# Optimization experiments

Measured on AMD Instinct MI355X. Metric: run time of the kernel, lower is better.

## Reference

```python
import jax, jax.numpy as jnp
import numpy as np

L = 3          # GRU layers
H = 512        # hidden_dim == latent_dim == atom_vocab_size (required for source to run)
V = 512        # atom_vocab_size
B = 16
S = 96


def setup_inputs() -> dict:
    key = jax.random.key(0)
    ks = jax.random.split(key, 16)
    p = lambda k, shape: jax.random.normal(k, shape, dtype=jnp.float32) * 0.05
    return {
        "z": jax.random.normal(ks[0], (B, H), dtype=jnp.float32),
        "W_l2h": p(ks[1], (H, H)), "b_l2h": p(ks[2], (H,)),
        # GRU weights, torch gate order (r, z, n); stored [in, 3H] so x @ W
        "W_ih": p(ks[3], (L, H, 3 * H)), "W_hh": p(ks[4], (L, H, 3 * H)),
        "b_ih": p(ks[5], (L, 3 * H)), "b_hh": p(ks[6], (L, 3 * H)),
        # atom predictor MLP
        "Wa1": p(ks[7], (H, H)), "ba1": p(ks[8], (H,)),
        "Wa2": p(ks[9], (H, V)), "ba2": p(ks[10], (V,)),
        # bond predictor MLP (in = 2*V = 2*H)
        "Wb1": p(ks[11], (2 * H, H)), "bb1": p(ks[12], (H,)),
        "Wb2": p(ks[13], (H, 4)), "bb2": p(ks[14], (4,)),
        "target_length": S,
    }


def _gru_cell(hl, x, Wih_l, Whh_l, bih_l, bhh_l):
    gi = x @ Wih_l + bih_l          # [B, 3H]
    gh = hl @ Whh_l + bhh_l         # [B, 3H]
    ir, iz, inn = jnp.split(gi, 3, axis=-1)
    hr, hz, hn = jnp.split(gh, 3, axis=-1)
    r = jax.nn.sigmoid(ir + hr)
    zg = jax.nn.sigmoid(iz + hz)
    n = jnp.tanh(inn + r * hn)
    return (1.0 - zg) * n + zg * hl


def reference(z, W_l2h, b_l2h, W_ih, W_hh, b_ih, b_hh,
              Wa1, ba1, Wa2, ba2, Wb1, bb1, Wb2, bb2, target_length):
    batch = z.shape[0]
    seq_len = target_length
    h0 = z @ W_l2h + b_l2h                         # [B, H]
    hidden0 = jnp.broadcast_to(h0[None], (L, batch, H))  # repeat over layers

    x0 = jnp.zeros((batch, H), dtype=z.dtype)      # decoder input is zeros each step

    def step(hs, _):
        x = x0
        new = []
        for l in range(L):
            hl = _gru_cell(hs[l], x, W_ih[l], W_hh[l], b_ih[l], b_hh[l])
            new.append(hl)
            x = hl                                  # no inter-layer dropout (eval)
        logits = jax.nn.relu(x @ Wa1 + ba1) @ Wa2 + ba2   # [B, V]
        return jnp.stack(new), logits

    _, atoms = jax.lax.scan(step, hidden0, None, length=seq_len)  # [S, B, V]
    atoms = atoms.transpose(1, 0, 2)                # [B, S, V]
    atom_indices = jnp.argmax(atoms, axis=-1)       # argmax(softmax) == argmax(logits)

    # all-pairs bond MLP, vectorized: split first linear to avoid [B,S,S,2V] concat
    e_i = atoms @ Wb1[:V]                           # [B, S, H] (contribution of atom i)
    e_j = atoms @ Wb1[V:]                           # [B, S, H] (contribution of atom j)
    hp = jax.nn.relu(e_i[:, :, None, :] + e_j[:, None, :, :] + bb1)  # [B, S, S, H]
    edge = hp @ Wb2 + bb2                           # [B, S, S, 4]
    mask = 1.0 - jnp.eye(seq_len, dtype=edge.dtype)  # i == j entries stay zero
    edge = edge * mask[None, :, :, None]
    return atom_indices, edge
```

## Files before the change

kernel.cpp:

```cpp
#include <hip/hip_runtime.h>
#include <math.h>

#define H    512
#define TH3  1536
#define GRID 224

#define WS_STATE(l,p) ((size_t)((l)*3+(p)) * 8192)
#define WS_A1(p)      ((size_t)73728 + (size_t)(p)*8192)
#define WS_ATOMS      ((size_t)98304)
#define WS_E          ((size_t)884736)

__device__ __forceinline__ float sigm_(float x) { return 1.0f / (1.0f + expf(-x)); }

__device__ __forceinline__ float stampf(float x, unsigned b) {
    return __uint_as_float((__float_as_uint(x) & ~1u) | b);
}
__device__ __forceinline__ int lsb4ok(float4 v, unsigned e) {
    return ((__float_as_uint(v.x) & 1u) == e) & ((__float_as_uint(v.y) & 1u) == e) &
           ((__float_as_uint(v.z) & 1u) == e) & ((__float_as_uint(v.w) & 1u) == e);
}

__device__ __forceinline__ void ld_coh4(const float* p0, const float* p1,
                                        const float* p2, const float* p3,
                                        float4& a, float4& b, float4& c, float4& d)
{
    asm volatile(
        "global_load_dwordx4 %0, %4, off sc0 sc1\n\t"
        "global_load_dwordx4 %1, %5, off sc0 sc1\n\t"
        "global_load_dwordx4 %2, %6, off sc0 sc1\n\t"
        "global_load_dwordx4 %3, %7, off sc0 sc1\n\t"
        "s_waitcnt vmcnt(0)"
        : "=&v"(a), "=&v"(b), "=&v"(c), "=&v"(d)
        : "v"(p0), "v"(p1), "v"(p2), "v"(p3)
        : "memory");
}

__device__ __forceinline__ void ld_coh8(const float* p0, const float* p1,
                                        const float* p2, const float* p3,
                                        const float* p4, const float* p5,
                                        const float* p6, const float* p7,
                                        float4& a, float4& b, float4& c, float4& d,
                                        float4& e, float4& f, float4& g, float4& h)
{
    asm volatile(
        "global_load_dwordx4 %0, %8, off sc0 sc1\n\t"
        "global_load_dwordx4 %1, %9, off sc0 sc1\n\t"
        "global_load_dwordx4 %2, %10, off sc0 sc1\n\t"
        "global_load_dwordx4 %3, %11, off sc0 sc1\n\t"
        "global_load_dwordx4 %4, %12, off sc0 sc1\n\t"
        "global_load_dwordx4 %5, %13, off sc0 sc1\n\t"
        "global_load_dwordx4 %6, %14, off sc0 sc1\n\t"
        "global_load_dwordx4 %7, %15, off sc0 sc1\n\t"
        "s_waitcnt vmcnt(0)"
        : "=&v"(a), "=&v"(b), "=&v"(c), "=&v"(d),
          "=&v"(e), "=&v"(f), "=&v"(g), "=&v"(h)
        : "v"(p0), "v"(p1), "v"(p2), "v"(p3),
          "v"(p4), "v"(p5), "v"(p6), "v"(p7)
        : "memory");
}

__device__ __forceinline__ void st_coh1(float* p, float v) {
    asm volatile("global_store_dword %0, %1, off sc0 sc1" :: "v"(p), "v"(v) : "memory");
}

__device__ __forceinline__ void ld_coh_u32x2(const unsigned* p0, const unsigned* p1,
                                             unsigned& a, unsigned& b)
{
    asm volatile(
        "global_load_dword %0, %2, off sc0 sc1\n\t"
        "global_load_dword %1, %3, off sc0 sc1\n\t"
        "s_waitcnt vmcnt(0)"
        : "=&v"(a), "=&v"(b)
        : "v"(p0), "v"(p1)
        : "memory");
}

__device__ __forceinline__ void st_coh_u32(unsigned* p, unsigned v) {
    asm volatile("global_store_dword %0, %1, off sc0 sc1" :: "v"(p), "v"(v) : "memory");
}

__device__ __forceinline__ void vm_drain() {
    asm volatile("s_waitcnt vmcnt(0)" ::: "memory");
}

template<int CTRL>
__device__ __forceinline__ float dppmov(float v) {
    return __int_as_float(__builtin_amdgcn_update_dpp(
        0, __float_as_int(v), CTRL, 0xF, 0xF, true));
}
#define DPP_XOR1 0xB1
#define DPP_XOR2 0x4E
#define DPP_XOR8 0x128

template<int PAT>
__device__ __forceinline__ float swzf(float v) {
    return __int_as_float(__builtin_amdgcn_ds_swizzle(__float_as_int(v), PAT));
}
#define SWZ_XOR4  0x101F
#define SWZ_XOR16 0x401F

extern "C" __global__ __launch_bounds__(256)
void k_init(const float* __restrict__ z, const float* __restrict__ Wl2h,
            const float* __restrict__ bl2h, float* __restrict__ ws)
{
    if (blockIdx.x == 0)
        ((unsigned*)(ws + WS_E))[threadIdx.x] = 0u;
    const int t  = threadIdx.x;
    const int jl = t & 15, b = t >> 4;
    const int j  = blockIdx.x * 16 + jl;
    float acc = 0.f;
    #pragma unroll 4
    for (int k = 0; k < H; ++k)
        acc += z[b * H + k] * Wl2h[(size_t)k * H + j];
    acc += bl2h[j];

    const unsigned realLsb[3] = { 1u, 0u, 1u };
    const int preh[3][3] = { { 1, 0, -1 },
                             { -1, 0, 1 },
                             { 0, -1, 1 } };
    const unsigned preA1[3] = { 0u, 1u, 0u };
    #pragma unroll
    for (int l = 0; l < 3; ++l)
        #pragma unroll
        for (int p = 0; p < 3; ++p) {
            float v = (preh[l][p] < 0) ? stampf(acc, realLsb[l])
                                       : __uint_as_float((unsigned)preh[l][p]);
            ws[WS_STATE(l, p) + j * 16 + b] = v;
        }
    #pragma unroll
    for (int p = 0; p < 3; ++p)
        ws[WS_A1(p) + j * 16 + b] = __uint_as_float(preA1[p]);
}

__global__ __launch_bounds__(512, 2)
void k_gru(const float* __restrict__ W_ih, const float* __restrict__ W_hh,
           const float* __restrict__ b_ih, const float* __restrict__ b_hh,
           const float* __restrict__ Wa1,  const float* __restrict__ ba1,
           const float* __restrict__ Wa2,  const float* __restrict__ ba2,
           float* __restrict__ ws)
{
    __shared__ float sx[10240];
    __shared__ float sh[10240];
    __shared__ float red[768];
    unsigned* flags = (unsigned*)(ws + WS_E);

    const int bid = blockIdx.x;
    const int tid = threadIdx.x;

    int job, jbase;
    if      (bid < 32)  { job = 0; jbase = bid * 16; }
    else if (bid < 96)  { job = 1; jbase = (bid - 32) * 8; }
    else if (bid < 160) { job = 2; jbase = (bid - 96) * 8; }
    else if (bid < 192) { job = 3; jbase = (bid - 160) * 16; }
    else                { job = 4; jbase = (bid - 192) * 16; }

    const int ks = tid & 31;
    const int qh = (tid >> 5) & 1;
    const int cs = tid >> 6;

    int rs0, rc0;
    if      (job == 0) { rs0 = 0;   rc0 = 96;  }
    else if (job == 1) { rs0 = 32;  rc0 = 128; }
    else if (job == 2) { rs0 = 96;  rc0 = 96;  }
    else if (job == 3) { rs0 = 192; rc0 = 32;  }
    else               { rs0 = 0;   rc0 = 0;   }
    int fidl[2];
    #pragma unroll
    for (int e = 0; e < 2; ++e) {
        int idx = (tid & 63) + e * 64;
        fidl[e] = (idx < rc0) ? rs0 + idx : bid;
    }

    float w[6][16];
    if (job <= 2) {
        const float* Wsrc;
        int colbase;
        if (job == 0) { Wsrc = W_hh; colbase = jbase + cs * 2; }
        else {
            Wsrc = ((cs & 1) ? W_hh : W_ih) + (size_t)job * H * TH3;
            colbase = jbase + (cs >> 1) * 2;
        }
        #pragma unroll
        for (int f = 0; f < 6; ++f) {
            int g = f >> 1, c = f & 1;
            #pragma unroll
            for (int kk = 0; kk < 16; ++kk)
                w[f][kk] = Wsrc[(size_t)(kk * 32 + ks) * TH3 + g * 512 + colbase + c];
        }
    } else {
        const float* base = (job == 3) ? Wa1 : Wa2;
        int colbase = jbase + cs * 2;
        #pragma unroll
        for (int f = 0; f < 2; ++f)
            #pragma unroll
            for (int kk = 0; kk < 16; ++kk)
                w[f][kk] = base[(size_t)(kk * 32 + ks) * H + colbase + f];
    }

    float c_bi0 = 0, c_bi1 = 0, c_bi2 = 0, c_bh0 = 0, c_bh1 = 0, c_bh2 = 0;
    float hp = 0.f, c_ba = 0.f;
    if (job == 0 && tid < 256) {
        int b = tid & 15, j2 = tid >> 4, jc = jbase + j2;
        c_bi0 = b_ih[jc]; c_bi1 = b_ih[512 + jc]; c_bi2 = b_ih[1024 + jc];
        c_bh0 = b_hh[jc]; c_bh1 = b_hh[512 + jc]; c_bh2 = b_hh[1024 + jc];
        hp = ws[WS_STATE(0, 2) + jc * 16 + b];
    } else if ((job == 1 || job == 2) && tid < 128) {
        int b = tid & 15, j2 = tid >> 4, jc = jbase + j2;
        const float* bi  = b_ih + job * TH3;
        const float* bhh = b_hh + job * TH3;
        c_bi0 = bi[jc]; c_bi1 = bi[512 + jc]; c_bi2 = bi[1024 + jc];
        c_bh0 = bhh[jc]; c_bh1 = bhh[512 + jc]; c_bh2 = bhh[1024 + jc];
        hp = ws[WS_STATE(job, (job + 2) % 3) + jc * 16 + b];
    } else if (job == 3 && tid < 256) {
        c_ba = ba1[jbase + (tid >> 4)];
    } else if (job == 4 && tid < 256) {
        c_ba = ba2[jbase + (tid & 15)];
    }

    const int k0 = tid >> 2;
    const int q4 = (tid & 3) * 4;
    const bool b0 = (ks & 1), b1 = (ks & 2), b3 = (ks & 8), b4 = (ks & 16);

    for (int s = 0; s < 100; ++s) {
        const int rp = (s + 2) % 3, wp = s % 3;
        const int act = (s >= job && s <= 95 + job);

        if (act) {
            const unsigned expb = (unsigned)((s + 1) & 1);

            if (tid < 64 && s >= 2) {
                unsigned lim = (unsigned)(s - 1);
                for (;;) {
                    unsigned v0, v1;
                    ld_coh_u32x2(&flags[fidl[0]], &flags[fidl[1]], v0, v1);
                    int ok = (v0 >= lim) && (v1 >= lim);
                    if (__all(ok)) break;
                    __builtin_amdgcn_s_sleep(1);
                }
            }

            if (job == 1 || job == 2) {
                const float* sA = ws + WS_STATE(job - 1, rp);
                const float* sB = ws + WS_STATE(job, rp);
                float4 xa, xb, xc, xd, ha, hb, hc, hd;
                for (;;) {
                    ld_coh8(sA + 4 * tid, sA + 4 * (tid + 512),
                            sA + 4 * (tid + 1024), sA + 4 * (tid + 1536),
                            sB + 4 * tid, sB + 4 * (tid + 512),
                            sB + 4 * (tid + 1024), sB + 4 * (tid + 1536),
                            xa, xb, xc, xd, ha, hb, hc, hd);
                    int ok = lsb4ok(xa, expb) & lsb4ok(xb, expb) &
                             lsb4ok(xc, expb) & lsb4ok(xd, expb) &
                             lsb4ok(ha, expb) & lsb4ok(hb, expb) &
                             lsb4ok(hc, expb) & lsb4ok(hd, expb);
                    if (__all(ok)) break;
                    __builtin_amdgcn_s_sleep(1);
                }
                *(float4*)&sx[(k0      ) * 20 + q4] = xa;
                *(float4*)&sx[(k0 + 128) * 20 + q4] = xb;
                *(float4*)&sx[(k0 + 256) * 20 + q4] = xc;
                *(float4*)&sx[(k0 + 384) * 20 + q4] = xd;
                *(float4*)&sh[(k0      ) * 20 + q4] = ha;
                *(float4*)&sh[(k0 + 128) * 20 + q4] = hb;
                *(float4*)&sh[(k0 + 256) * 20 + q4] = hc;
                *(float4*)&sh[(k0 + 384) * 20 + q4] = hd;
            } else {
                const float* sA = (job == 0) ? (ws + WS_STATE(0, rp))
                                : (job == 3) ? (ws + WS_STATE(2, rp))
                                             : (ws + WS_A1(rp));
                float4 xa, xb, xc, xd;
                for (;;) {
                    ld_coh4(sA + 4 * tid, sA + 4 * (tid + 512),
                            sA + 4 * (tid + 1024), sA + 4 * (tid + 1536),
                            xa, xb, xc, xd);
                    int ok = lsb4ok(xa, expb) & lsb4ok(xb, expb) &
                             lsb4ok(xc, expb) & lsb4ok(xd, expb);
                    if (__all(ok)) break;
                    __builtin_amdgcn_s_sleep(1);
                }
                *(float4*)&sx[(k0      ) * 20 + q4] = xa;
                *(float4*)&sx[(k0 + 128) * 20 + q4] = xb;
                *(float4*)&sx[(k0 + 256) * 20 + q4] = xc;
                *(float4*)&sx[(k0 + 384) * 20 + q4] = xd;
            }
            __syncthreads();

            const int rowoff = 8 * qh;
            if (job <= 2) {
                const float* arr = (job != 0 && (cs & 1)) ? sh : sx;
                float acc[6][8];
                #pragma unroll
                for (int f = 0; f < 6; ++f)
                    #pragma unroll
                    for (int i = 0; i < 8; ++i) acc[f][i] = 0.f;
                #pragma unroll
                for (int kk = 0; kk < 16; ++kk) {
                    const float* p = arr + (kk * 32 + ks) * 20 + rowoff;
                    float4 v0 = *(const float4*)p;
                    float4 v1 = *(const float4*)(p + 4);
                    #pragma unroll
                    for (int f = 0; f < 6; ++f) {
                        float wv = w[f][kk];
                        acc[f][0] += wv * v0.x; acc[f][1] += wv * v0.y;
                        acc[f][2] += wv * v0.z; acc[f][3] += wv * v0.w;
                        acc[f][4] += wv * v1.x; acc[f][5] += wv * v1.y;
                        acc[f][6] += wv * v1.z; acc[f][7] += wv * v1.w;
                    }
                }
                float a[6];
                #pragma unroll
                for (int f = 0; f < 6; ++f) {
                    float t[4];
                    #pragma unroll
                    for (int j = 0; j < 4; ++j) {
                        float give = b0 ? acc[f][j] : acc[f][j + 4];
                        float recv = dppmov<DPP_XOR1>(give);
                        float keep = b0 ? acc[f][j + 4] : acc[f][j];
                        t[j] = keep + recv;
                    }
                    float u[2];
                    #pragma unroll
                    for (int j = 0; j < 2; ++j) {
                        float give = b1 ? t[j] : t[j + 2];
                        float recv = dppmov<DPP_XOR2>(give);
                        float keep = b1 ? t[j + 2] : t[j];
                        u[j] = keep + recv;
                    }
                    {
                        float give = b3 ? u[0] : u[1];
                        float recv = dppmov<DPP_XOR8>(give);
                        float keep = b3 ? u[1] : u[0];
                        a[f] = keep + recv;
                    }
                }
                #pragma unroll
                for (int f = 0; f < 6; ++f) a[f] += swzf<SWZ_XOR4>(a[f]);
                float r[3];
                #pragma unroll
                for (int i = 0; i < 3; ++i) {
                    float give = b4 ? a[i] : a[i + 3];
                    float recv = swzf<SWZ_XOR16>(give);
                    float keep = b4 ? a[i + 3] : a[i];
                    r[i] = keep + recv;
                }
                if (!(ks & 4)) {
                    int bl = ((ks & 1) << 2) | (ks & 2) | ((ks >> 3) & 1);
                    int bb = qh * 8 + bl;
                    int fb3 = ((ks >> 4) & 1) * 3;
                    #pragma unroll
                    for (int i = 0; i < 3; ++i) {
                        int f = fb3 + i, g = f >> 1, c = f & 1;
                        int idx = (job == 0)
                            ? g * 256 + (cs * 2 + c) * 16 + bb
                            : (cs & 1) * 384 + g * 128 + ((cs >> 1) * 2 + c) * 16 + bb;
                        red[idx] = r[i];
                    }
                }
            } else {
                float acc[2][8];
                #pragma unroll
                for (int f = 0; f < 2; ++f)
                    #pragma unroll
                    for (int i = 0; i < 8; ++i) acc[f][i] = 0.f;
                #pragma unroll
                for (int kk = 0; kk < 16; ++kk) {
                    const float* p = sx + (kk * 32 + ks) * 20 + rowoff;
                    float4 v0 = *(const float4*)p;
                    float4 v1 = *(const float4*)(p + 4);
                    #pragma unroll
                    for (int f = 0; f < 2; ++f) {
                        float wv = w[f][kk];
                        acc[f][0] += wv * v0.x; acc[f][1] += wv * v0.y;
                        acc[f][2] += wv * v0.z; acc[f][3] += wv * v0.w;
                        acc[f][4] += wv * v1.x; acc[f][5] += wv * v1.y;
                        acc[f][6] += wv * v1.z; acc[f][7] += wv * v1.w;
                    }
                }
                float a[2];
                #pragma unroll
                for (int f = 0; f < 2; ++f) {
                    float t[4];
                    #pragma unroll
                    for (int j = 0; j < 4; ++j) {
                        float give = b0 ? acc[f][j] : acc[f][j + 4];
                        float recv = dppmov<DPP_XOR1>(give);
                        float keep = b0 ? acc[f][j + 4] : acc[f][j];
                        t[j] = keep + recv;
                    }
                    float u[2];
                    #pragma unroll
                    for (int j = 0; j < 2; ++j) {
                        float give = b1 ? t[j] : t[j + 2];
                        float recv = dppmov<DPP_XOR2>(give);
                        float keep = b1 ? t[j + 2] : t[j];
                        u[j] = keep + recv;
                    }
                    float give = b3 ? u[0] : u[1];
                    float recv = dppmov<DPP_XOR8>(give);
                    float keep = b3 ? u[1] : u[0];
                    a[f] = keep + recv;
                }
                a[0] += swzf<SWZ_XOR4>(a[0]);
                a[1] += swzf<SWZ_XOR4>(a[1]);
                float give = b4 ? a[0] : a[1];
                float recv = swzf<SWZ_XOR16>(give);
                float keep = b4 ? a[1] : a[0];
                float r0 = keep + recv;
                if (!(ks & 4)) {
                    int bl = ((ks & 1) << 2) | (ks & 2) | ((ks >> 3) & 1);
                    int bb = qh * 8 + bl;
                    int fb = (ks >> 4) & 1;
                    red[(cs * 2 + fb) * 16 + bb] = r0;
                }
            }
            __syncthreads();

            const unsigned myb = (unsigned)(s & 1);
            if (job == 0) {
                if (tid < 256) {
                    int b = tid & 15, j2 = tid >> 4, jc = jbase + j2;
                    float g0 = red[       j2 * 16 + b];
                    float g1 = red[256  + j2 * 16 + b];
                    float g2 = red[512  + j2 * 16 + b];
                    float r  = sigm_(c_bi0 + g0 + c_bh0);
                    float zg = sigm_(c_bi1 + g1 + c_bh1);
                    float n  = tanhf(c_bi2 + r * (g2 + c_bh2));
                    float hn = (1.f - zg) * n + zg * hp;
                    hp = hn;
                    st_coh1(&ws[WS_STATE(0, wp) + jc * 16 + b], stampf(hn, myb));
                }
            } else if (job <= 2) {
                if (tid < 128) {
                    int b = tid & 15, j2 = tid >> 4, jc = jbase + j2;
                    float gi0 = red[        j2 * 16 + b], gh0 = red[384 +       j2 * 16 + b];
                    float gi1 = red[128  +  j2 * 16 + b], gh1 = red[384 + 128 + j2 * 16 + b];
                    float gi2 = red[256  +  j2 * 16 + b], gh2 = red[384 + 256 + j2 * 16 + b];
                    float r  = sigm_(gi0 + c_bi0 + gh0 + c_bh0);
                    float zg = sigm_(gi1 + c_bi1 + gh1 + c_bh1);
                    float n  = tanhf(gi2 + c_bi2 + r * (gh2 + c_bh2));
                    float hn = (1.f - zg) * n + zg * hp;
                    hp = hn;
                    st_coh1(&ws[WS_STATE(job, wp) + jc * 16 + b], stampf(hn, myb));
                }
            } else if (job == 3) {
                if (tid < 256) {
                    int b = tid & 15, j2 = tid >> 4, jc = jbase + j2;
                    float v = red[j2 * 16 + b] + c_ba;
                    st_coh1(&ws[WS_A1(wp) + jc * 16 + b], stampf(fmaxf(v, 0.f), myb));
                }
            } else {
                if (tid < 256) {
                    int j2 = tid & 15, b = tid >> 4, jc = jbase + j2;
                    float v = red[j2 * 16 + b] + c_ba;
                    ws[WS_ATOMS + ((size_t)(s - 4) * 16 + b) * H + jc] = v;
                }
            }
        }

        vm_drain();
        __syncthreads();
        if (tid == 0) st_coh_u32(&flags[bid], (unsigned)(s + 1));
    }
}

extern "C" __global__ __launch_bounds__(256)
void k_argmax(const float* __restrict__ ws, float* __restrict__ out)
{
    const int t = blockIdx.x;
    const int wv = threadIdx.x >> 6, lane = threadIdx.x & 63;
    for (int b = wv; b < 16; b += 4) {
        const float* row = ws + WS_ATOMS + ((size_t)t * 16 + b) * H;
        float mx = -3.4028235e38f; int mi = 0;
        #pragma unroll
        for (int c = 0; c < 8; ++c) {
            int idx = lane + c * 64;
            float v = row[idx];
            if (v > mx) { mx = v; mi = idx; }
        }
        #pragma unroll
        for (int off = 32; off >= 1; off >>= 1) {
            float omx = __shfl_down(mx, off);
            int   omi = __shfl_down(mi, off);
            if (omx > mx || (omx == mx && omi < mi)) { mx = omx; mi = omi; }
        }
        if (lane == 0) out[b * 96 + t] = (float)mi;
    }
}

extern "C" __global__ __launch_bounds__(256)
void k_eij(const float* __restrict__ Wb1, const float* __restrict__ bb1,
           float* __restrict__ ws)
{
    __shared__ float aT[8192];
    const int bid = blockIdx.x;
    const int t = bid >> 4, m = (bid >> 3) & 1, ct = bid & 7;
    const int tid = threadIdx.x;
    const float* atoms = ws + WS_ATOMS;
    for (int f = tid; f < 2048; f += 256) {
        int b = f >> 7, kq = f & 127;
        float4 v = ((const float4*)(atoms + ((size_t)(t * 16 + b)) * H))[kq];
        aT[(kq * 4 + 0) * 16 + b] = v.x;
        aT[(kq * 4 + 1) * 16 + b] = v.y;
        aT[(kq * 4 + 2) * 16 + b] = v.z;
        aT[(kq * 4 + 3) * 16 + b] = v.w;
    }
    __syncthreads();
    const int c = tid & 63, rq = tid >> 6;
    const int col = ct * 64 + c;
    const float* Wp = Wb1 + (size_t)m * H * H + col;
    float a0 = 0, a1 = 0, a2 = 0, a3 = 0;
    #pragma unroll 8
    for (int k = 0; k < 512; ++k) {
        float  wv = Wp[(size_t)k * H];
        float4 av = *(const float4*)&aT[k * 16 + rq * 4];
        a0 += av.x * wv; a1 += av.y * wv; a2 += av.z * wv; a3 += av.w * wv;
    }
    float bb = (m == 0) ? bb1[col] : 0.f;
    a0 += bb; a1 += bb; a2 += bb; a3 += bb;
    float* eb = ws + WS_E + (size_t)(m * 16) * 96 * H;
    eb[((size_t)(rq * 4 + 0) * 96 + t) * H + col] = a0;
    eb[((size_t)(rq * 4 + 1) * 96 + t) * H + col] = a1;
    eb[((size_t)(rq * 4 + 2) * 96 + t) * H + col] = a2;
    eb[((size_t)(rq * 4 + 3) * 96 + t) * H + col] = a3;
}

extern "C" __global__ __launch_bounds__(256)
void k_edge(const float* __restrict__ Wb2, const float* __restrict__ bb2,
            const float* __restrict__ ws, float* __restrict__ out)
{
    __shared__ float ls[32][260];
    __shared__ float wsm[2048];
    const int bid = blockIdx.x;
    const int b = bid / 36, r6 = bid % 36, it = r6 / 6, jt = r6 % 6;
    const int tid = threadIdx.x;
    const int ip = tid & 15, jp = tid >> 4;
    float acc0 = 0, acc1 = 0, acc2 = 0, acc3 = 0;

    for (int f = tid; f < 2048; f += 256)
        wsm[f] = Wb2[f];

    for (int ph = 0; ph < 2; ++ph) {
        __syncthreads();
        for (int f = tid; f < 2048; f += 256) {
            int r = f >> 6, c4 = f & 63;
            const float* src = (r < 16)
                ? ws + WS_E + ((size_t)b * 96 + it * 16 + r) * H
                : ws + WS_E + ((size_t)(16 + b) * 96 + jt * 16 + (r - 16)) * H;
            float4 v = *(const float4*)(src + ph * 256 + c4 * 4);
            *(float4*)&ls[r][c4 * 4] = v;
        }
        __syncthreads();
        const float* wb = &wsm[ph * 1024];
        #pragma unroll 2
        for (int hh = 0; hh < 256; hh += 4) {
            float4 ei = *(const float4*)&ls[ip][hh];
            float4 ej = *(const float4*)&ls[16 + jp][hh];
            float4 w0 = *(const float4*)(wb + (size_t)hh * 4);
            float4 w1 = *(const float4*)(wb + (size_t)hh * 4 + 4);
            float4 w2 = *(const float4*)(wb + (size_t)hh * 4 + 8);
            float4 w3 = *(const float4*)(wb + (size_t)hh * 4 + 12);
            float v;
            v = fmaxf(ei.x + ej.x, 0.f); acc0 += v * w0.x; acc1 += v * w0.y; acc2 += v * w0.z; acc3 += v * w0.w;
            v = fmaxf(ei.y + ej.y, 0.f); acc0 += v * w1.x; acc1 += v * w1.y; acc2 += v * w1.z; acc3 += v * w1.w;
            v = fmaxf(ei.z + ej.z, 0.f); acc0 += v * w2.x; acc1 += v * w2.y; acc2 += v * w2.z; acc3 += v * w2.w;
            v = fmaxf(ei.w + ej.w, 0.f); acc0 += v * w3.x; acc1 += v * w3.y; acc2 += v * w3.z; acc3 += v * w3.w;
        }
    }
    const int i = it * 16 + ip, j = jt * 16 + jp;
    float4 o;
    if (i == j) { o.x = 0.f; o.y = 0.f; o.z = 0.f; o.w = 0.f; }
    else { o.x = acc0 + bb2[0]; o.y = acc1 + bb2[1]; o.z = acc2 + bb2[2]; o.w = acc3 + bb2[3]; }
    *(float4*)(out + 1536 + (((size_t)b * 96 + i) * 96 + j) * 4) = o;
}

extern "C" void kernel_launch(void* const* d_in, const int* in_sizes, int n_in,
                              void* d_out, int out_size, void* d_ws, size_t ws_size,
                              hipStream_t stream)
{
    const float* z    = (const float*)d_in[0];
    const float* Wl2h = (const float*)d_in[1];
    const float* bl2h = (const float*)d_in[2];
    const float* W_ih = (const float*)d_in[3];
    const float* W_hh = (const float*)d_in[4];
    const float* b_ih = (const float*)d_in[5];
    const float* b_hh = (const float*)d_in[6];
    const float* Wa1  = (const float*)d_in[7];
    const float* ba1  = (const float*)d_in[8];
    const float* Wa2  = (const float*)d_in[9];
    const float* ba2  = (const float*)d_in[10];
    const float* Wb1  = (const float*)d_in[11];
    const float* bb1  = (const float*)d_in[12];
    const float* Wb2  = (const float*)d_in[13];
    const float* bb2  = (const float*)d_in[14];
    float* out = (float*)d_out;
    float* ws  = (float*)d_ws;

    hipLaunchKernelGGL(k_init, dim3(32), dim3(256), 0, stream, z, Wl2h, bl2h, ws);

    hipLaunchKernelGGL(k_gru, dim3(GRID), dim3(512), 0, stream,
                       W_ih, W_hh, b_ih, b_hh, Wa1, ba1, Wa2, ba2, ws);

    hipLaunchKernelGGL(k_argmax, dim3(96), dim3(256), 0, stream, ws, out);
    hipLaunchKernelGGL(k_eij, dim3(1536), dim3(256), 0, stream, Wb1, bb1, ws);
    hipLaunchKernelGGL(k_edge, dim3(576), dim3(256), 0, stream, Wb2, bb2, ws, out);
}
```

Baseline: 850.1 us.

## Rebalance persistent GRU blocks and prefetch input-layer state one step early

Reassigns the persistent-kernel block roles. Layer 0 now gets 64 blocks of 8 columns, and the atom MLP stages get 16 blocks of 32 columns each. Layers 1 and 2 now stage the previous layer's hidden state into shared memory during the prior iteration, so the input-side matvec can start before the recurrent state arrives. To support this, the per-layer schedule is staggered to 102 steps with new parity stamps and initial buffer patterns, and the reduction buffer is enlarged. The aim is to shorten the critical path of the pipelined recurrence, at the cost of more complex cross-block synchronisation and a longer pipeline fill.

```diff
diff --git a/kernel.cpp b/kernel.cpp
--- a/kernel.cpp
+++ b/kernel.cpp
@@ -35,28 +35,11 @@
         : "memory");
 }
 
-__device__ __forceinline__ void ld_coh8(const float* p0, const float* p1,
-                                        const float* p2, const float* p3,
-                                        const float* p4, const float* p5,
-                                        const float* p6, const float* p7,
-                                        float4& a, float4& b, float4& c, float4& d,
-                                        float4& e, float4& f, float4& g, float4& h)
-{
+__device__ __forceinline__ void ld_coh_u32(const unsigned* p, unsigned& a) {
     asm volatile(
-        "global_load_dwordx4 %0, %8, off sc0 sc1\n\t"
-        "global_load_dwordx4 %1, %9, off sc0 sc1\n\t"
-        "global_load_dwordx4 %2, %10, off sc0 sc1\n\t"
-        "global_load_dwordx4 %3, %11, off sc0 sc1\n\t"
-        "global_load_dwordx4 %4, %12, off sc0 sc1\n\t"
-        "global_load_dwordx4 %5, %13, off sc0 sc1\n\t"
-        "global_load_dwordx4 %6, %14, off sc0 sc1\n\t"
-        "global_load_dwordx4 %7, %15, off sc0 sc1\n\t"
+        "global_load_dword %0, %1, off sc0 sc1\n\t"
         "s_waitcnt vmcnt(0)"
-        : "=&v"(a), "=&v"(b), "=&v"(c), "=&v"(d),
-          "=&v"(e), "=&v"(f), "=&v"(g), "=&v"(h)
-        : "v"(p0), "v"(p1), "v"(p2), "v"(p3),
-          "v"(p4), "v"(p5), "v"(p6), "v"(p7)
-        : "memory");
+        : "=&v"(a) : "v"(p) : "memory");
 }
 
 __device__ __forceinline__ void st_coh1(float* p, float v) {
@@ -114,19 +97,18 @@
         acc += z[b * H + k] * Wl2h[(size_t)k * H + j];
     acc += bl2h[j];
 
-    const unsigned realLsb[3] = { 1u, 0u, 1u };
     const int preh[3][3] = { { 1, 0, -1 },
-                             { -1, 0, 1 },
-                             { 0, -1, 1 } };
-    const unsigned preA1[3] = { 0u, 1u, 0u };
+                             { 0, -1, 1 },
+                             { -1, 1, 0 } };
     #pragma unroll
     for (int l = 0; l < 3; ++l)
         #pragma unroll
         for (int p = 0; p < 3; ++p) {
-            float v = (preh[l][p] < 0) ? stampf(acc, realLsb[l])
+            float v = (preh[l][p] < 0) ? stampf(acc, 1u)
                                        : __uint_as_float((unsigned)preh[l][p]);
             ws[WS_STATE(l, p) + j * 16 + b] = v;
         }
+    const unsigned preA1[3] = { 1u, 0u, 0u };
     #pragma unroll
     for (int p = 0; p < 3; ++p)
         ws[WS_A1(p) + j * 16 + b] = __uint_as_float(preA1[p]);
@@ -141,28 +123,27 @@
 {
     __shared__ float sx[10240];
     __shared__ float sh[10240];
-    __shared__ float red[768];
+    __shared__ float red[1536];
     unsigned* flags = (unsigned*)(ws + WS_E);
 
     const int bid = blockIdx.x;
     const int tid = threadIdx.x;
 
     int job, jbase;
-    if      (bid < 32)  { job = 0; jbase = bid * 16; }
-    else if (bid < 96)  { job = 1; jbase = (bid - 32) * 8; }
-    else if (bid < 160) { job = 2; jbase = (bid - 96) * 8; }
-    else if (bid < 192) { job = 3; jbase = (bid - 160) * 16; }
-    else                { job = 4; jbase = (bid - 192) * 16; }
+    if      (bid < 64)  { job = 0; jbase = bid * 8; }
+    else if (bid < 128) { job = 1; jbase = (bid - 64) * 8; }
+    else if (bid < 192) { job = 2; jbase = (bid - 128) * 8; }
+    else if (bid < 208) { job = 3; jbase = (bid - 192) * 32; }
+    else                { job = 4; jbase = (bid - 208) * 32; }
 
     const int ks = tid & 31;
-    const int qh = (tid >> 5) & 1;
     const int cs = tid >> 6;
 
     int rs0, rc0;
-    if      (job == 0) { rs0 = 0;   rc0 = 96;  }
-    else if (job == 1) { rs0 = 32;  rc0 = 128; }
-    else if (job == 2) { rs0 = 96;  rc0 = 96;  }
-    else if (job == 3) { rs0 = 192; rc0 = 32;  }
+    if      (job == 0) { rs0 = 0;   rc0 = 128; }
+    else if (job == 1) { rs0 = 64;  rc0 = 128; }
+    else if (job == 2) { rs0 = 128; rc0 = 80;  }
+    else if (job == 3) { rs0 = 208; rc0 = 16;  }
     else               { rs0 = 0;   rc0 = 0;   }
     int fidl[2];
     #pragma unroll
@@ -173,25 +154,25 @@
 
     float w[6][16];
     if (job <= 2) {
-        const float* Wsrc;
-        int colbase;
-        if (job == 0) { Wsrc = W_hh; colbase = jbase + cs * 2; }
-        else {
-            Wsrc = ((cs & 1) ? W_hh : W_ih) + (size_t)job * H * TH3;
-            colbase = jbase + (cs >> 1) * 2;
-        }
+        const int khalf = cs & 1, cpair = cs >> 1;
+        const int colbase = jbase + cpair * 2;
+        const float* WB = W_hh + (size_t)job * H * TH3;
+        const float* WA = W_ih + (size_t)job * H * TH3;
         #pragma unroll
         for (int f = 0; f < 6; ++f) {
             int g = f >> 1, c = f & 1;
             #pragma unroll
-            for (int kk = 0; kk < 16; ++kk)
-                w[f][kk] = Wsrc[(size_t)(kk * 32 + ks) * TH3 + g * 512 + colbase + c];
+            for (int kk = 0; kk < 8; ++kk) {
+                size_t ro = (size_t)(khalf * 256 + kk * 32 + ks) * TH3 + g * 512 + colbase + c;
+                w[f][8 + kk] = WB[ro];
+                if (job != 0) w[f][kk] = WA[ro];
+            }
         }
     } else {
         const float* base = (job == 3) ? Wa1 : Wa2;
-        int colbase = jbase + cs * 2;
-        #pragma unroll
-        for (int f = 0; f < 2; ++f)
+        const int colbase = jbase + cs * 4;
+        #pragma unroll
+        for (int f = 0; f < 4; ++f)
             #pragma unroll
             for (int kk = 0; kk < 16; ++kk)
                 w[f][kk] = base[(size_t)(kk * 32 + ks) * H + colbase + f];
@@ -199,229 +180,239 @@
 
     float c_bi0 = 0, c_bi1 = 0, c_bi2 = 0, c_bh0 = 0, c_bh1 = 0, c_bh2 = 0;
     float hp = 0.f, c_ba = 0.f;
-    if (job == 0 && tid < 256) {
-        int b = tid & 15, j2 = tid >> 4, jc = jbase + j2;
-        c_bi0 = b_ih[jc]; c_bi1 = b_ih[512 + jc]; c_bi2 = b_ih[1024 + jc];
-        c_bh0 = b_hh[jc]; c_bh1 = b_hh[512 + jc]; c_bh2 = b_hh[1024 + jc];
-        hp = ws[WS_STATE(0, 2) + jc * 16 + b];
-    } else if ((job == 1 || job == 2) && tid < 128) {
-        int b = tid & 15, j2 = tid >> 4, jc = jbase + j2;
-        const float* bi  = b_ih + job * TH3;
-        const float* bhh = b_hh + job * TH3;
-        c_bi0 = bi[jc]; c_bi1 = bi[512 + jc]; c_bi2 = bi[1024 + jc];
-        c_bh0 = bhh[jc]; c_bh1 = bhh[512 + jc]; c_bh2 = bhh[1024 + jc];
-        hp = ws[WS_STATE(job, (job + 2) % 3) + jc * 16 + b];
-    } else if (job == 3 && tid < 256) {
+    if (job <= 2) {
+        if (tid < 128) {
+            int b = tid & 15, j2 = tid >> 4, jc = jbase + j2;
+            const float* bi  = b_ih + (size_t)job * TH3;
+            const float* bhh = b_hh + (size_t)job * TH3;
+            c_bi0 = bi[jc]; c_bi1 = bi[512 + jc]; c_bi2 = bi[1024 + jc];
+            c_bh0 = bhh[jc]; c_bh1 = bhh[512 + jc]; c_bh2 = bhh[1024 + jc];
+            const int hpp = (job == 0) ? 2 : (job == 1) ? 1 : 0;
+            hp = ws[WS_STATE(job, hpp) + jc * 16 + b];
+        }
+    } else if (job == 3) {
         c_ba = ba1[jbase + (tid >> 4)];
-    } else if (job == 4 && tid < 256) {
-        c_ba = ba2[jbase + (tid & 15)];
-    }
-
-    const int k0 = tid >> 2;
-    const int q4 = (tid & 3) * 4;
-    const bool b0 = (ks & 1), b1 = (ks & 2), b3 = (ks & 8), b4 = (ks & 16);
-
-    for (int s = 0; s < 100; ++s) {
+    } else {
+        c_ba = ba2[jbase + (tid & 31)];
+    }
+
+    auto stage32k = [&](const float* src, unsigned eb, float* dst, int precheck) {
+        if (precheck) {
+            const unsigned* cp = (const unsigned*)src + (size_t)tid * 16;
+            for (;;) {
+                unsigned v; ld_coh_u32(cp, v);
+                if (__all((int)((v & 1u) == eb))) break;
+                __builtin_amdgcn_s_sleep(1);
+            }
+        }
+        const int k0 = tid >> 2, q4 = (tid & 3) * 4;
+        float4 a, b, c, d;
+        for (;;) {
+            ld_coh4(src + 4 * tid, src + 4 * (tid + 512),
+                    src + 4 * (tid + 1024), src + 4 * (tid + 1536), a, b, c, d);
+            if (__all(lsb4ok(a, eb) & lsb4ok(b, eb) & lsb4ok(c, eb) & lsb4ok(d, eb)))
+                break;
+            __builtin_amdgcn_s_sleep(1);
+        }
+        *(float4*)&dst[(k0      ) * 20 + q4] = a;
+        *(float4*)&dst[(k0 + 128) * 20 + q4] = b;
+        *(float4*)&dst[(k0 + 256) * 20 + q4] = c;
+        *(float4*)&dst[(k0 + 384) * 20 + q4] = d;
+    };
+
+    auto mv6 = [&](const float* arr, int wo, int redbase) {
+        const int qh = (tid >> 5) & 1;
+        const int khalf = cs & 1, cpair = cs >> 1;
+        const int rowoff = 8 * qh;
+        const bool b0 = (ks & 1), b1 = (ks & 2), b3 = (ks & 8), b4 = (ks & 16);
+        const float* base = arr + khalf * (256 * 20);
+        float acc[6][8];
+        #pragma unroll
+        for (int f = 0; f < 6; ++f)
+            #pragma unroll
+            for (int i = 0; i < 8; ++i) acc[f][i] = 0.f;
+        #pragma unroll
+        for (int kk = 0; kk < 8; ++kk) {
+            const float* p = base + (kk * 32 + ks) * 20 + rowoff;
+            float4 v0 = *(const float4*)p;
+            float4 v1 = *(const float4*)(p + 4);
+            #pragma unroll
+            for (int f = 0; f < 6; ++f) {
+                float wv = w[f][wo + kk];
+                acc[f][0] += wv * v0.x; acc[f][1] += wv * v0.y;
+                acc[f][2] += wv * v0.z; acc[f][3] += wv * v0.w;
+                acc[f][4] += wv * v1.x; acc[f][5] += wv * v1.y;
+                acc[f][6] += wv * v1.z; acc[f][7] += wv * v1.w;
+            }
+        }
+        float a[6];
+        #pragma unroll
+        for (int f = 0; f < 6; ++f) {
+            float t[4];
+            #pragma unroll
+            for (int j = 0; j < 4; ++j) {
+                float give = b0 ? acc[f][j] : acc[f][j + 4];
+                float recv = dppmov<DPP_XOR1>(give);
+                float keep = b0 ? acc[f][j + 4] : acc[f][j];
+                t[j] = keep + recv;
+            }
+            float u[2];
+            #pragma unroll
+            for (int j = 0; j < 2; ++j) {
+                float give = b1 ? t[j] : t[j + 2];
+                float recv = dppmov<DPP_XOR2>(give);
+                float keep = b1 ? t[j + 2] : t[j];
+                u[j] = keep + recv;
+            }
+            float give = b3 ? u[0] : u[1];
+            float recv = dppmov<DPP_XOR8>(give);
+            float keep = b3 ? u[1] : u[0];
+            a[f] = keep + recv;
+        }
+        #pragma unroll
+        for (int f = 0; f < 6; ++f) a[f] += swzf<SWZ_XOR4>(a[f]);
+        float r[3];
+        #pragma unroll
+        for (int i = 0; i < 3; ++i) {
+            float give = b4 ? a[i] : a[i + 3];
+            float recv = swzf<SWZ_XOR16>(give);
+            float keep = b4 ? a[i + 3] : a[i];
+            r[i] = keep + recv;
+        }
+        if (!(ks & 4)) {
+            int bl = ((ks & 1) << 2) | (ks & 2) | ((ks >> 3) & 1);
+            int bb = ((tid >> 5) & 1) * 8 + bl;
+            int fb3 = ((ks >> 4) & 1) * 3;
+            #pragma unroll
+            for (int i = 0; i < 3; ++i) {
+                int f = fb3 + i, g = f >> 1, c = f & 1;
+                red[redbase + (cs & 1) * 384 + g * 128 + ((cs >> 1) * 2 + c) * 16 + bb] = r[i];
+            }
+        }
+    };
+
+    auto mv4 = [&](const float* arr) {
+        const int qh = (tid >> 5) & 1;
+        const int rowoff = 8 * qh;
+        const bool b0 = (ks & 1), b1 = (ks & 2), b3 = (ks & 8), b4 = (ks & 16);
+        float acc[4][8];
+        #pragma unroll
+        for (int f = 0; f < 4; ++f)
+            #pragma unroll
+            for (int i = 0; i < 8; ++i) acc[f][i] = 0.f;
+        #pragma unroll
+        for (int kk = 0; kk < 16; ++kk) {
+            const float* p = arr + (kk * 32 + ks) * 20 + rowoff;
+            float4 v0 = *(const float4*)p;
+            float4 v1 = *(const float4*)(p + 4);
+            #pragma unroll
+            for (int f = 0; f < 4; ++f) {
+                float wv = w[f][kk];
+                acc[f][0] += wv * v0.x; acc[f][1] += wv * v0.y;
+                acc[f][2] += wv * v0.z; acc[f][3] += wv * v0.w;
+                acc[f][4] += wv * v1.x; acc[f][5] += wv * v1.y;
+                acc[f][6] += wv * v1.z; acc[f][7] += wv * v1.w;
+            }
+        }
+        float a[4];
+        #pragma unroll
+        for (int f = 0; f < 4; ++f) {
+            float t[4];
+            #pragma unroll
+            for (int j = 0; j < 4; ++j) {
+                float give = b0 ? acc[f][j] : acc[f][j + 4];
+                float recv = dppmov<DPP_XOR1>(give);
+                float keep = b0 ? acc[f][j + 4] : acc[f][j];
+                t[j] = keep + recv;
+            }
+            float u[2];
+            #pragma unroll
+            for (int j = 0; j < 2; ++j) {
+                float give = b1 ? t[j] : t[j + 2];
+                float recv = dppmov<DPP_XOR2>(give);
+                float keep = b1 ? t[j + 2] : t[j];
+                u[j] = keep + recv;
+            }
+            float give = b3 ? u[0] : u[1];
+            float recv = dppmov<DPP_XOR8>(give);
+            float keep = b3 ? u[1] : u[0];
+            a[f] = keep + recv;
+        }
+        #pragma unroll
+        for (int f = 0; f < 4; ++f) a[f] += swzf<SWZ_XOR4>(a[f]);
+        float r[2];
+        #pragma unroll
+        for (int i = 0; i < 2; ++i) {
+            float give = b4 ? a[i] : a[i + 2];
+            float recv = swzf<SWZ_XOR16>(give);
+            float keep = b4 ? a[i + 2] : a[i];
+            r[i] = keep + recv;
+        }
+        if (!(ks & 4)) {
+            int bl = ((ks & 1) << 2) | (ks & 2) | ((ks >> 3) & 1);
+            int bb = ((tid >> 5) & 1) * 8 + bl;
+            int f2 = ((ks >> 4) & 1) * 2;
+            #pragma unroll
+            for (int i = 0; i < 2; ++i)
+                red[(cs * 4 + f2 + i) * 16 + bb] = r[i];
+        }
+    };
+
+    for (int s = 0; s < 102; ++s) {
         const int rp = (s + 2) % 3, wp = s % 3;
-        const int act = (s >= job && s <= 95 + job);
+        const unsigned expb = (unsigned)((s + 1) & 1);
+        const unsigned myb  = (unsigned)(s & 1);
+        int act;
+        if      (job == 0) act = (s <= 95);
+        else if (job == 1) act = (s >= 2 && s <= 97);
+        else if (job == 2) act = (s >= 4 && s <= 99);
+        else if (job == 3) act = (s >= 5 && s <= 100);
+        else               act = (s >= 6 && s <= 101);
 
         if (act) {
-            const unsigned expb = (unsigned)((s + 1) & 1);
-
             if (tid < 64 && s >= 2) {
                 unsigned lim = (unsigned)(s - 1);
                 for (;;) {
                     unsigned v0, v1;
                     ld_coh_u32x2(&flags[fidl[0]], &flags[fidl[1]], v0, v1);
-                    int ok = (v0 >= lim) && (v1 >= lim);
-                    if (__all(ok)) break;
+                    if (__all((int)((v0 >= lim) & (v1 >= lim)))) break;
                     __builtin_amdgcn_s_sleep(1);
                 }
             }
 
             if (job == 1 || job == 2) {
-                const float* sA = ws + WS_STATE(job - 1, rp);
-                const float* sB = ws + WS_STATE(job, rp);
-                float4 xa, xb, xc, xd, ha, hb, hc, hd;
-                for (;;) {
-                    ld_coh8(sA + 4 * tid, sA + 4 * (tid + 512),
-                            sA + 4 * (tid + 1024), sA + 4 * (tid + 1536),
-                            sB + 4 * tid, sB + 4 * (tid + 512),
-                            sB + 4 * (tid + 1024), sB + 4 * (tid + 1536),
-                            xa, xb, xc, xd, ha, hb, hc, hd);
-                    int ok = lsb4ok(xa, expb) & lsb4ok(xb, expb) &
-                             lsb4ok(xc, expb) & lsb4ok(xd, expb) &
-                             lsb4ok(ha, expb) & lsb4ok(hb, expb) &
-                             lsb4ok(hc, expb) & lsb4ok(hd, expb);
-                    if (__all(ok)) break;
-                    __builtin_amdgcn_s_sleep(1);
+                mv6(sx, 0, 0);
+                stage32k(ws + WS_STATE(job, rp), expb, sh, 0);
+                __syncthreads();
+                mv6(sh, 8, 768);
+                __syncthreads();
+                if (tid < 128) {
+                    int b = tid & 15, jc = jbase + (tid >> 4);
+                    int o = tid;
+                    float gi0 = red[o]        + red[384 + o];
+                    float gi1 = red[128 + o]  + red[512 + o];
+                    float gi2 = red[256 + o]  + red[640 + o];
+                    float gh0 = red[768 + o]  + red[1152 + o];
+                    float gh1 = red[896 + o]  + red[1280 + o];
+                    float gh2 = red[1024 + o] + red[1408 + o];
+                    float r  = sigm_(gi0 + c_bi0 + gh0 + c_bh0);
+                    float zg = sigm_(gi1 + c_bi1 + gh1 + c_bh1);
+                    float n  = tanhf(gi2 + c_bi2 + r * (gh2 + c_bh2));
+                    float hn = (1.f - zg) * n + zg * hp;
+                    hp = hn;
+                    st_coh1(&ws[WS_STATE(job, wp) + jc * 16 + b], stampf(hn, myb));
                 }
-                *(float4*)&sx[(k0      ) * 20 + q4] = xa;
-                *(float4*)&sx[(k0 + 128) * 20 + q4] = xb;
-                *(float4*)&sx[(k0 + 256) * 20 + q4] = xc;
-                *(float4*)&sx[(k0 + 384) * 20 + q4] = xd;
-                *(float4*)&sh[(k0      ) * 20 + q4] = ha;
-                *(float4*)&sh[(k0 + 128) * 20 + q4] = hb;
-                *(float4*)&sh[(k0 + 256) * 20 + q4] = hc;
-                *(float4*)&sh[(k0 + 384) * 20 + q4] = hd;
-            } else {
-                const float* sA = (job == 0) ? (ws + WS_STATE(0, rp))
-                                : (job == 3) ? (ws + WS_STATE(2, rp))
-                                             : (ws + WS_A1(rp));
-                float4 xa, xb, xc, xd;
-                for (;;) {
-                    ld_coh4(sA + 4 * tid, sA + 4 * (tid + 512),
-                            sA + 4 * (tid + 1024), sA + 4 * (tid + 1536),
-                            xa, xb, xc, xd);
-                    int ok = lsb4ok(xa, expb) & lsb4ok(xb, expb) &
-                             lsb4ok(xc, expb) & lsb4ok(xd, expb);
-                    if (__all(ok)) break;
-                    __builtin_amdgcn_s_sleep(1);
-                }
-                *(float4*)&sx[(k0      ) * 20 + q4] = xa;
-                *(float4*)&sx[(k0 + 128) * 20 + q4] = xb;
-                *(float4*)&sx[(k0 + 256) * 20 + q4] = xc;
-                *(float4*)&sx[(k0 + 384) * 20 + q4] = xd;
-            }
-            __syncthreads();
-
-            const int rowoff = 8 * qh;
-            if (job <= 2) {
-                const float* arr = (job != 0 && (cs & 1)) ? sh : sx;
-                float acc[6][8];
-                #pragma unroll
-                for (int f = 0; f < 6; ++f)
-                    #pragma unroll
-                    for (int i = 0; i < 8; ++i) acc[f][i] = 0.f;
-                #pragma unroll
-                for (int kk = 0; kk < 16; ++kk) {
-                    const float* p = arr + (kk * 32 + ks) * 20 + rowoff;
-                    float4 v0 = *(const float4*)p;
-                    float4 v1 = *(const float4*)(p + 4);
-                    #pragma unroll
-                    for (int f = 0; f < 6; ++f) {
-                        float wv = w[f][kk];
-                        acc[f][0] += wv * v0.x; acc[f][1] += wv * v0.y;
-                        acc[f][2] += wv * v0.z; acc[f][3] += wv * v0.w;
-                        acc[f][4] += wv * v1.x; acc[f][5] += wv * v1.y;
-                        acc[f][6] += wv * v1.z; acc[f][7] += wv * v1.w;
-                    }
-                }
-                float a[6];
-                #pragma unroll
-                for (int f = 0; f < 6; ++f) {
-                    float t[4];
-                    #pragma unroll
-                    for (int j = 0; j < 4; ++j) {
-                        float give = b0 ? acc[f][j] : acc[f][j + 4];
-                        float recv = dppmov<DPP_XOR1>(give);
-                        float keep = b0 ? acc[f][j + 4] : acc[f][j];
-                        t[j] = keep + recv;
-                    }
-                    float u[2];
-                    #pragma unroll
-                    for (int j = 0; j < 2; ++j) {
-                        float give = b1 ? t[j] : t[j + 2];
-                        float recv = dppmov<DPP_XOR2>(give);
-                        float keep = b1 ? t[j + 2] : t[j];
-                        u[j] = keep + recv;
-                    }
-                    {
-                        float give = b3 ? u[0] : u[1];
-                        float recv = dppmov<DPP_XOR8>(give);
-                        float keep = b3 ? u[1] : u[0];
-                        a[f] = keep + recv;
-                    }
-                }
-                #pragma unroll
-                for (int f = 0; f < 6; ++f) a[f] += swzf<SWZ_XOR4>(a[f]);
-                float r[3];
-                #pragma unroll
-                for (int i = 0; i < 3; ++i) {
-                    float give = b4 ? a[i] : a[i + 3];
-                    float recv = swzf<SWZ_XOR16>(give);
-                    float keep = b4 ? a[i + 3] : a[i];
-                    r[i] = keep + recv;
-                }
-                if (!(ks & 4)) {
-                    int bl = ((ks & 1) << 2) | (ks & 2) | ((ks >> 3) & 1);
-                    int bb = qh * 8 + bl;
-                    int fb3 = ((ks >> 4) & 1) * 3;
-                    #pragma unroll
-                    for (int i = 0; i < 3; ++i) {
-                        int f = fb3 + i, g = f >> 1, c = f & 1;
-                        int idx = (job == 0)
-                            ? g * 256 + (cs * 2 + c) * 16 + bb
-                            : (cs & 1) * 384 + g * 128 + ((cs >> 1) * 2 + c) * 16 + bb;
-                        red[idx] = r[i];
-                    }
-                }
-            } else {
-                float acc[2][8];
-                #pragma unroll
-                for (int f = 0; f < 2; ++f)
-                    #pragma unroll
-                    for (int i = 0; i < 8; ++i) acc[f][i] = 0.f;
-                #pragma unroll
-                for (int kk = 0; kk < 16; ++kk) {
-                    const float* p = sx + (kk * 32 + ks) * 20 + rowoff;
-                    float4 v0 = *(const float4*)p;
-                    float4 v1 = *(const float4*)(p + 4);
-                    #pragma unroll
-                    for (int f = 0; f < 2; ++f) {
-                        float wv = w[f][kk];
-                        acc[f][0] += wv * v0.x; acc[f][1] += wv * v0.y;
-                        acc[f][2] += wv * v0.z; acc[f][3] += wv * v0.w;
-                        acc[f][4] += wv * v1.x; acc[f][5] += wv * v1.y;
-                        acc[f][6] += wv * v1.z; acc[f][7] += wv * v1.w;
-                    }
-                }
-                float a[2];
-                #pragma unroll
-                for (int f = 0; f < 2; ++f) {
-                    float t[4];
-                    #pragma unroll
-                    for (int j = 0; j < 4; ++j) {
-                        float give = b0 ? acc[f][j] : acc[f][j + 4];
-                        float recv = dppmov<DPP_XOR1>(give);
-                        float keep = b0 ? acc[f][j + 4] : acc[f][j];
-                        t[j] = keep + recv;
-                    }
-                    float u[2];
-                    #pragma unroll
-                    for (int j = 0; j < 2; ++j) {
-                        float give = b1 ? t[j] : t[j + 2];
-                        float recv = dppmov<DPP_XOR2>(give);
-                        float keep = b1 ? t[j + 2] : t[j];
-                        u[j] = keep + recv;
-                    }
-                    float give = b3 ? u[0] : u[1];
-                    float recv = dppmov<DPP_XOR8>(give);
-                    float keep = b3 ? u[1] : u[0];
-                    a[f] = keep + recv;
-                }
-                a[0] += swzf<SWZ_XOR4>(a[0]);
-                a[1] += swzf<SWZ_XOR4>(a[1]);
-                float give = b4 ? a[0] : a[1];
-                float recv = swzf<SWZ_XOR16>(give);
-                float keep = b4 ? a[1] : a[0];
-                float r0 = keep + recv;
-                if (!(ks & 4)) {
-                    int bl = ((ks & 1) << 2) | (ks & 2) | ((ks >> 3) & 1);
-                    int bb = qh * 8 + bl;
-                    int fb = (ks >> 4) & 1;
-                    red[(cs * 2 + fb) * 16 + bb] = r0;
-                }
-            }
-            __syncthreads();
-
-            const unsigned myb = (unsigned)(s & 1);
-            if (job == 0) {
-                if (tid < 256) {
-                    int b = tid & 15, j2 = tid >> 4, jc = jbase + j2;
-                    float g0 = red[       j2 * 16 + b];
-                    float g1 = red[256  + j2 * 16 + b];
-                    float g2 = red[512  + j2 * 16 + b];
+            } else if (job == 0) {
+                stage32k(ws + WS_STATE(0, rp), expb, sx, 1);
+                __syncthreads();
+                mv6(sx, 8, 768);
+                __syncthreads();
+                if (tid < 128) {
+                    int b = tid & 15, jc = jbase + (tid >> 4);
+                    int o = tid;
+                    float g0 = red[768 + o]  + red[1152 + o];
+                    float g1 = red[896 + o]  + red[1280 + o];
+                    float g2 = red[1024 + o] + red[1408 + o];
                     float r  = sigm_(c_bi0 + g0 + c_bh0);
                     float zg = sigm_(c_bi1 + g1 + c_bh1);
                     float n  = tanhf(c_bi2 + r * (g2 + c_bh2));
@@ -429,32 +420,29 @@
                     hp = hn;
                     st_coh1(&ws[WS_STATE(0, wp) + jc * 16 + b], stampf(hn, myb));
                 }
-            } else if (job <= 2) {
-                if (tid < 128) {
-                    int b = tid & 15, j2 = tid >> 4, jc = jbase + j2;
-                    float gi0 = red[        j2 * 16 + b], gh0 = red[384 +       j2 * 16 + b];
-                    float gi1 = red[128  +  j2 * 16 + b], gh1 = red[384 + 128 + j2 * 16 + b];
-                    float gi2 = red[256  +  j2 * 16 + b], gh2 = red[384 + 256 + j2 * 16 + b];
-                    float r  = sigm_(gi0 + c_bi0 + gh0 + c_bh0);
-                    float zg = sigm_(gi1 + c_bi1 + gh1 + c_bh1);
-                    float n  = tanhf(gi2 + c_bi2 + r * (gh2 + c_bh2));
-                    float hn = (1.f - zg) * n + zg * hp;
-                    hp = hn;
-                    st_coh1(&ws[WS_STATE(job, wp) + jc * 16 + b], stampf(hn, myb));
-                }
-            } else if (job == 3) {
-                if (tid < 256) {
+            } else {
+                const float* srcp = (job == 3) ? (ws + WS_STATE(2, rp))
+                                               : (ws + WS_A1(rp));
+                stage32k(srcp, expb, sx, 1);
+                __syncthreads();
+                mv4(sx);
+                __syncthreads();
+                if (job == 3) {
                     int b = tid & 15, j2 = tid >> 4, jc = jbase + j2;
                     float v = red[j2 * 16 + b] + c_ba;
                     st_coh1(&ws[WS_A1(wp) + jc * 16 + b], stampf(fmaxf(v, 0.f), myb));
+                } else {
+                    int j2 = tid & 31, b = tid >> 5, jc = jbase + j2;
+                    float v = red[j2 * 16 + b] + c_ba;
+                    ws[WS_ATOMS + ((size_t)(s - 6) * 16 + b) * H + jc] = v;
                 }
-            } else {
-                if (tid < 256) {
-                    int j2 = tid & 15, b = tid >> 4, jc = jbase + j2;
-                    float v = red[j2 * 16 + b] + c_ba;
-                    ws[WS_ATOMS + ((size_t)(s - 4) * 16 + b) * H + jc] = v;
-                }
-            }
+            }
+        }
+
+        if (job == 1 || job == 2) {
+            const int s0 = (job == 1) ? 1 : 3;
+            if (s >= s0 && s <= s0 + 95)
+                stage32k(ws + WS_STATE(job - 1, rp), expb, sx, 0);
         }
 
         vm_drain();
```

Result: no change. 860.0 us (+1.2%).
